# Kernel tuning notes

Measured on AMD Instinct MI355X. Metric: run time of the kernel, lower is better.

## Reference

```python
import jax, jax.numpy as jnp
import numpy as np

WS = 7           # window side
N = WS * WS      # tokens per window = 49
DIM = 384
H = 12
HD = DIM // H    # 32
BW = 2048        # num_windows * batch
NW = 4           # windows per image (mask batch)
SCALE = 1.0 / float(np.sqrt(HD))


def _rel_index():
    coords = np.stack(np.meshgrid(np.arange(WS), np.arange(WS), indexing='ij'))  # (2,7,7)
    flat = coords.reshape(2, -1)                      # (2,49)
    rel = flat[:, :, None] - flat[:, None, :]         # (2,49,49)
    rel = rel.transpose(1, 2, 0).copy()               # (49,49,2)
    rel[..., 0] += WS - 1
    rel[..., 1] += WS - 1
    rel[..., 0] *= 2 * WS - 1
    return jnp.asarray(rel.sum(-1), dtype=jnp.int32)  # (49,49)


def setup_inputs() -> dict:
    key = jax.random.key(0)
    ks = jax.random.split(key, 16)
    f32 = jnp.float32
    se = jax.random.normal(ks[0], (BW, N, DIM), dtype=f32)
    de = jax.random.normal(ks[1], (BW, N, DIM), dtype=f32)
    mask = jnp.where(jax.random.uniform(ks[2], (NW, N, N)) < 0.1, f32(-1e9), f32(0.0))
    s = 0.02
    w_v_se = jax.random.normal(ks[3], (DIM, DIM), dtype=f32) * s
    b_v_se = jnp.zeros((DIM,), dtype=f32)
    w_qkv = jax.random.normal(ks[4], (3 * DIM, DIM), dtype=f32) * s
    b_qkv = jnp.zeros((3 * DIM,), dtype=f32)
    w_proj_se = jax.random.normal(ks[5], (DIM, DIM), dtype=f32) * s
    b_proj_se = jnp.zeros((DIM,), dtype=f32)
    w_proj_de = jax.random.normal(ks[6], (DIM, DIM), dtype=f32) * s
    b_proj_de = jnp.zeros((DIM,), dtype=f32)
    rpb = jax.random.normal(ks[7], ((2 * WS - 1) ** 2, H), dtype=f32) * s  # (169,12)
    rel_idx = _rel_index()
    return {
        'se': se, 'de': de, 'mask': mask,
        'w_v_se': w_v_se, 'b_v_se': b_v_se,
        'w_qkv': w_qkv, 'b_qkv': b_qkv,
        'w_proj_se': w_proj_se, 'b_proj_se': b_proj_se,
        'w_proj_de': w_proj_de, 'b_proj_de': b_proj_de,
        'rpb': rpb, 'rel_idx': rel_idx,
    }


def reference(se, de, mask, w_v_se, b_v_se, w_qkv, b_qkv,
              w_proj_se, b_proj_se, w_proj_de, b_proj_de, rpb, rel_idx):
    B_, N_, C = se.shape
    # qkv from de (coa=False branch)
    qkv = (de @ w_qkv.T + b_qkv).reshape(B_, N_, 3, H, HD).transpose(2, 0, 3, 1, 4)
    q, k, v_de = qkv[0], qkv[1], qkv[2]                 # (B_,H,N,HD)
    v_se = (se @ w_v_se.T + b_v_se).reshape(B_, N_, H, HD).transpose(0, 2, 1, 3)
    attn = jnp.einsum('bhnd,bhmd->bhnm', q * SCALE, k)  # (B_,H,N,N)
    bias = rpb[rel_idx].transpose(2, 0, 1)              # (H,N,N)
    attn = attn + bias[None]
    # add window mask: view as (B, nW, H, N, N)
    attn = attn.reshape(B_ // NW, NW, H, N_, N_) + mask[None, :, None]
    attn = jax.nn.softmax(attn.reshape(B_, H, N_, N_), axis=-1)
    se_o = jnp.einsum('bhnm,bhmd->bnhd', attn, v_se).reshape(B_, N_, C)
    de_o = jnp.einsum('bhnm,bhmd->bnhd', attn, v_de).reshape(B_, N_, C)
    se_o = se_o @ w_proj_se.T + b_proj_se
    de_o = de_o @ w_proj_de.T + b_proj_de
    return (se_o, de_o)
```

## Files before the change

### kernel.cpp

```cpp
#include <hip/hip_runtime.h>

typedef _Float16 f16;
typedef __attribute__((ext_vector_type(8))) _Float16 f16x8;
typedef __attribute__((ext_vector_type(4))) _Float16 f16x4;
typedef __attribute__((ext_vector_type(4))) float f32x4;

#define MFMA16(a, b, c) __builtin_amdgcn_mfma_f32_16x16x32_f16(a, b, c, 0, 0, 0)

#define SCALE_F 0.17677669529663687f
#define NHEAD 12
#define NTOK 49
#define NBW 2048

__global__ void cast_f32_to_f16(const float* __restrict__ in, f16* __restrict__ out, int n4) {
    int i0 = blockIdx.x * 256 + threadIdx.x;
    int stride = gridDim.x * 256;
    for (int i = i0; i < n4; i += stride) {
        f32x4 v = ((const f32x4*)in)[i];
        f16x4 o;
#pragma unroll
        for (int e = 0; e < 4; ++e) o[e] = (f16)v[e];
        ((f16x4*)out)[i] = o;
    }
}

__global__ void prep_bm(const float* __restrict__ rpb, const int* __restrict__ rel_idx,
                        const float* __restrict__ mask, float* __restrict__ bm) {
    int blk = blockIdx.x;
    int w4 = blk / NHEAD, h = blk - w4 * NHEAD;
    for (int idx = threadIdx.x; idx < 4096; idx += 64) {
        int r = idx >> 6, c = idx & 63;
        float v = -1e30f;
        if (r < NTOK && c < NTOK)
            v = rpb[rel_idx[r * NTOK + c] * NHEAD + h] + mask[(w4 * NTOK + r) * NTOK + c];
        bm[(size_t)blk * 4096 + idx] = v;
    }
}

template <typename OUT_T>
__global__ __launch_bounds__(256) void gemm_bt(const f16* __restrict__ A, const f16* __restrict__ B,
                                               const float* __restrict__ bias, OUT_T* __restrict__ C,
                                               int M, int N, int K) {
    __shared__ __align__(16) f16 As[128 * 64];
    __shared__ __align__(16) f16 Bs[128 * 64];
    const int m0 = blockIdx.y * 128, n0 = blockIdx.x * 128;
    const int tid = threadIdx.x;
    const int w = tid >> 6, l = tid & 63;
    const int wm = w >> 1, wn = w & 1;
    const int lr = l & 15, lg = l >> 4;
    const int sp = l & 7;

    f32x4 acc[4][4] = {};

    for (int k0 = 0; k0 < K; k0 += 64) {
        __syncthreads();
#pragma unroll
        for (int it = 0; it < 4; ++it) {
            int row = w * 32 + it * 8 + (l >> 3);
            int gchunk = sp ^ (row & 7);
            const f16* gA = A + (size_t)(m0 + row) * K + k0 + gchunk * 8;
            const f16* gB = B + (size_t)(n0 + row) * K + k0 + gchunk * 8;
            f16* lA = As + (w * 32 + it * 8) * 64;
            f16* lB = Bs + (w * 32 + it * 8) * 64;
            __builtin_amdgcn_global_load_lds((const __attribute__((address_space(1))) void*)gA,
                                             (__attribute__((address_space(3))) void*)lA, 16, 0, 0);
            __builtin_amdgcn_global_load_lds((const __attribute__((address_space(1))) void*)gB,
                                             (__attribute__((address_space(3))) void*)lB, 16, 0, 0);
        }
        __syncthreads();
#pragma unroll
        for (int ks = 0; ks < 2; ++ks) {
            f16x8 af[4], bfr[4];
#pragma unroll
            for (int mi = 0; mi < 4; ++mi) {
                int r = 64 * wm + 16 * mi + lr;
                int chunk = (lg + 4 * ks) ^ (r & 7);
                af[mi] = *(const f16x8*)(As + r * 64 + chunk * 8);
            }
#pragma unroll
            for (int ni = 0; ni < 4; ++ni) {
                int r = 64 * wn + 16 * ni + lr;
                int chunk = (lg + 4 * ks) ^ (r & 7);
                bfr[ni] = *(const f16x8*)(Bs + r * 64 + chunk * 8);
            }
#pragma unroll
            for (int mi = 0; mi < 4; ++mi)
#pragma unroll
                for (int ni = 0; ni < 4; ++ni)
                    acc[mi][ni] = MFMA16(af[mi], bfr[ni], acc[mi][ni]);
        }
    }
#pragma unroll
    for (int mi = 0; mi < 4; ++mi) {
#pragma unroll
        for (int ni = 0; ni < 4; ++ni) {
            int col = n0 + 64 * wn + 16 * ni + lr;
            float bv = bias[col];
#pragma unroll
            for (int reg = 0; reg < 4; ++reg) {
                int row = m0 + 64 * wm + 16 * mi + 4 * lg + reg;
                C[(size_t)row * N + col] = (OUT_T)(acc[mi][ni][reg] + bv);
            }
        }
    }
}

__global__ __launch_bounds__(64) void attn_kernel(const f16* __restrict__ qkv,
                                                  const f16* __restrict__ vse,
                                                  const float* __restrict__ bm_all,
                                                  f16* __restrict__ att_se, f16* __restrict__ att_de) {
    __shared__ __align__(16) f16 Vts[2][32 * 64];
    __shared__ __align__(16) f16 Ps[64 * 64];

    const int bh = blockIdx.x;
    const int b = bh / NHEAD, h = bh - b * NHEAD;
    const int l = threadIdx.x;
    const int lr = l & 15, lg = l >> 4;
    const size_t wbase = (size_t)b * NTOK;

    for (int idx = l; idx < 2 * NTOK * 4; idx += 64) {
        int s = idx >= NTOK * 4;
        int t = idx - s * NTOK * 4;
        int j = t >> 2, part = t & 3;
        const f16* src = s ? (qkv + (wbase + j) * 1152 + 768 + h * 32 + part * 8)
                           : (vse + (wbase + j) * 384 + h * 32 + part * 8);
        f16x8 v = *(const f16x8*)src;
#pragma unroll
        for (int e = 0; e < 8; ++e) {
            int d = part * 8 + e;
            Vts[s][(d << 6) + (j ^ ((d & 7) << 3))] = v[e];
        }
    }
    for (int idx = l; idx < 2 * 32 * 15; idx += 64) {
        int s = idx / 480;
        int t = idx - s * 480;
        int d = t / 15, j = NTOK + (t - d * 15);
        Vts[s][(d << 6) + (j ^ ((d & 7) << 3))] = (f16)0.f;
    }

    const size_t MAXROW = (size_t)NBW * NTOK - 1;
    f16x8 qa[4], kb[4];
#pragma unroll
    for (int mi = 0; mi < 4; ++mi) {
        size_t gi = wbase + 16 * mi + lr;
        if (gi > MAXROW) gi = MAXROW;
        qa[mi] = *(const f16x8*)(qkv + gi * 1152 + h * 32 + lg * 8);
    }
#pragma unroll
    for (int ni = 0; ni < 4; ++ni) {
        size_t gj = wbase + 16 * ni + lr;
        if (gj > MAXROW) gj = MAXROW;
        kb[ni] = *(const f16x8*)(qkv + gj * 1152 + 384 + h * 32 + lg * 8);
    }
    const f32x4 zero4 = {0.f, 0.f, 0.f, 0.f};
    f32x4 S[4][4];
#pragma unroll
    for (int mi = 0; mi < 4; ++mi)
#pragma unroll
        for (int ni = 0; ni < 4; ++ni)
            S[mi][ni] = MFMA16(qa[mi], kb[ni], zero4);

    const float* bmp = bm_all + (size_t)((b & 3) * NHEAD + h) * 4096;
#pragma unroll
    for (int mi = 0; mi < 4; ++mi) {
#pragma unroll
        for (int reg = 0; reg < 4; ++reg) {
            int r = 16 * mi + 4 * lg + reg;
            float v[4];
#pragma unroll
            for (int ni = 0; ni < 4; ++ni)
                v[ni] = S[mi][ni][reg] * SCALE_F + bmp[(r << 6) + 16 * ni + lr];
            float mx = fmaxf(fmaxf(v[0], v[1]), fmaxf(v[2], v[3]));
#pragma unroll
            for (int off = 1; off < 16; off <<= 1) mx = fmaxf(mx, __shfl_xor(mx, off));
            float e[4];
            float sm = 0.f;
#pragma unroll
            for (int ni = 0; ni < 4; ++ni) {
                e[ni] = __expf(v[ni] - mx);
                sm += e[ni];
            }
#pragma unroll
            for (int off = 1; off < 16; off <<= 1) sm += __shfl_xor(sm, off);
            float inv = 1.f / sm;
#pragma unroll
            for (int ni = 0; ni < 4; ++ni)
                Ps[(r << 6) + ((16 * ni + lr) ^ ((r & 7) << 3))] = (f16)(e[ni] * inv);
        }
    }
    __syncthreads();

    f32x4 o[2][4][2] = {};
#pragma unroll
    for (int ks = 0; ks < 2; ++ks) {
        f16x8 pa[4];
#pragma unroll
        for (int mi = 0; mi < 4; ++mi) {
            int r = 16 * mi + lr;
            pa[mi] = *(const f16x8*)(Ps + (r << 6) + ((8 * lg + 32 * ks) ^ ((r & 7) << 3)));
        }
#pragma unroll
        for (int s = 0; s < 2; ++s) {
#pragma unroll
            for (int ni = 0; ni < 2; ++ni) {
                int d = 16 * ni + lr;
                f16x8 vb = *(const f16x8*)(Vts[s] + (d << 6) + ((8 * lg + 32 * ks) ^ ((d & 7) << 3)));
#pragma unroll
                for (int mi = 0; mi < 4; ++mi) o[s][mi][ni] = MFMA16(pa[mi], vb, o[s][mi][ni]);
            }
        }
    }
#pragma unroll
    for (int s = 0; s < 2; ++s) {
        f16* dst = s ? att_de : att_se;
#pragma unroll
        for (int mi = 0; mi < 4; ++mi) {
#pragma unroll
            for (int reg = 0; reg < 4; ++reg) {
                int r = 16 * mi + 4 * lg + reg;
                if (r < NTOK) {
#pragma unroll
                    for (int ni = 0; ni < 2; ++ni)
                        dst[(wbase + r) * 384 + h * 32 + 16 * ni + lr] = (f16)o[s][mi][ni][reg];
                }
            }
        }
    }
}

extern "C" void kernel_launch(void* const* d_in, const int* in_sizes, int n_in,
                              void* d_out, int out_size, void* d_ws, size_t ws_size,
                              hipStream_t stream) {
    const float* se = (const float*)d_in[0];
    const float* de = (const float*)d_in[1];
    const float* mask = (const float*)d_in[2];
    const float* w_v_se = (const float*)d_in[3];
    const float* b_v_se = (const float*)d_in[4];
    const float* w_qkv = (const float*)d_in[5];
    const float* b_qkv = (const float*)d_in[6];
    const float* w_proj_se = (const float*)d_in[7];
    const float* b_proj_se = (const float*)d_in[8];
    const float* w_proj_de = (const float*)d_in[9];
    const float* b_proj_de = (const float*)d_in[10];
    const float* rpb = (const float*)d_in[11];
    const int* rel_idx = (const int*)d_in[12];

    const size_t SE_ELEMS = (size_t)NBW * NTOK * 384;

    char* ws = (char*)d_ws;
    f16* de_h = (f16*)(ws);
    f16* se_h = (f16*)(ws + 77070336);
    f16* qkv_h = (f16*)(ws + 154140672);
    f16* vse_h = (f16*)(ws + 385351680);
    f16* wqkv_h = (f16*)(ws + 462422016);
    f16* wvse_h = (f16*)(ws + 463306752);
    f16* wpse_h = (f16*)(ws + 463601664);
    f16* wpde_h = (f16*)(ws + 463896576);
    float* bm = (float*)(ws + 464191488);

    auto cast = [&](const float* in, f16* out, size_t n) {
        int n4 = (int)(n / 4);
        int blocks = (n4 + 255) / 256;
        if (blocks > 2048) blocks = 2048;
        cast_f32_to_f16<<<blocks, 256, 0, stream>>>(in, out, n4);
    };
    cast(de, de_h, SE_ELEMS);
    cast(se, se_h, SE_ELEMS);
    cast(w_qkv, wqkv_h, (size_t)1152 * 384);
    cast(w_v_se, wvse_h, (size_t)384 * 384);
    cast(w_proj_se, wpse_h, (size_t)384 * 384);
    cast(w_proj_de, wpde_h, (size_t)384 * 384);

    prep_bm<<<48, 64, 0, stream>>>(rpb, rel_idx, mask, bm);

    gemm_bt<f16><<<dim3(9, 784), 256, 0, stream>>>(de_h, wqkv_h, b_qkv, qkv_h, 100352, 1152, 384);
    gemm_bt<f16><<<dim3(3, 784), 256, 0, stream>>>(se_h, wvse_h, b_v_se, vse_h, 100352, 384, 384);

    attn_kernel<<<NBW * NHEAD, 64, 0, stream>>>(qkv_h, vse_h, bm, de_h, se_h);

    gemm_bt<float><<<dim3(3, 784), 256, 0, stream>>>(de_h, wpse_h, b_proj_se, (float*)d_out, 100352, 384, 384);
    gemm_bt<float><<<dim3(3, 784), 256, 0, stream>>>(se_h, wpde_h, b_proj_de, (float*)d_out + SE_ELEMS, 100352,
                                                     384, 384);
}
```

Before: 724.3 us.

## Read V directly from global in attention and remap GEMM workgroups

The attention kernel no longer stages and transposes both V matrices into LDS. Instead each lane gathers its V fragment with eight strided 2-byte global loads right before the PV MFMAs, which removes the LDS transpose-and-pad pass and its shared memory. The change also drops the row clamping on Q/K loads, adds s_setprio around the MFMA bursts, and permutes the GEMM block index so consecutive blocks spread across 8 groups, for better cache locality. The costs are uncoalesced scalar global loads for V. Padding rows 49–63 now read the next window's data, or memory past the buffer for the last window, and rely on zeroed probabilities to cancel them, which is unsafe if those values are NaN or Inf.

```diff
diff --git a/kernel.cpp b/kernel.cpp
--- a/kernel.cpp
+++ b/kernel.cpp
@@ -43,7 +43,10 @@
                                                int M, int N, int K) {
     __shared__ __align__(16) f16 As[128 * 64];
     __shared__ __align__(16) f16 Bs[128 * 64];
-    const int m0 = blockIdx.y * 128, n0 = blockIdx.x * 128;
+    const int nwg = gridDim.x * gridDim.y;
+    int wg = blockIdx.y * gridDim.x + blockIdx.x;
+    wg = (wg & 7) * (nwg >> 3) + (wg >> 3);
+    const int m0 = (wg / gridDim.x) * 128, n0 = (wg % gridDim.x) * 128;
     const int tid = threadIdx.x;
     const int w = tid >> 6, l = tid & 63;
     const int wm = w >> 1, wn = w & 1;
@@ -109,7 +112,6 @@
                                                   const f16* __restrict__ vse,
                                                   const float* __restrict__ bm_all,
                                                   f16* __restrict__ att_se, f16* __restrict__ att_de) {
-    __shared__ __align__(16) f16 Vts[2][32 * 64];
     __shared__ __align__(16) f16 Ps[64 * 64];
 
     const int bh = blockIdx.x;
@@ -118,47 +120,23 @@
     const int lr = l & 15, lg = l >> 4;
     const size_t wbase = (size_t)b * NTOK;
 
-    for (int idx = l; idx < 2 * NTOK * 4; idx += 64) {
-        int s = idx >= NTOK * 4;
-        int t = idx - s * NTOK * 4;
-        int j = t >> 2, part = t & 3;
-        const f16* src = s ? (qkv + (wbase + j) * 1152 + 768 + h * 32 + part * 8)
-                           : (vse + (wbase + j) * 384 + h * 32 + part * 8);
-        f16x8 v = *(const f16x8*)src;
-#pragma unroll
-        for (int e = 0; e < 8; ++e) {
-            int d = part * 8 + e;
-            Vts[s][(d << 6) + (j ^ ((d & 7) << 3))] = v[e];
-        }
-    }
-    for (int idx = l; idx < 2 * 32 * 15; idx += 64) {
-        int s = idx / 480;
-        int t = idx - s * 480;
-        int d = t / 15, j = NTOK + (t - d * 15);
-        Vts[s][(d << 6) + (j ^ ((d & 7) << 3))] = (f16)0.f;
-    }
-
-    const size_t MAXROW = (size_t)NBW * NTOK - 1;
     f16x8 qa[4], kb[4];
 #pragma unroll
-    for (int mi = 0; mi < 4; ++mi) {
-        size_t gi = wbase + 16 * mi + lr;
-        if (gi > MAXROW) gi = MAXROW;
-        qa[mi] = *(const f16x8*)(qkv + gi * 1152 + h * 32 + lg * 8);
-    }
-#pragma unroll
-    for (int ni = 0; ni < 4; ++ni) {
-        size_t gj = wbase + 16 * ni + lr;
-        if (gj > MAXROW) gj = MAXROW;
-        kb[ni] = *(const f16x8*)(qkv + gj * 1152 + 384 + h * 32 + lg * 8);
-    }
+    for (int mi = 0; mi < 4; ++mi)
+        qa[mi] = *(const f16x8*)(qkv + (wbase + 16 * mi + lr) * 1152 + h * 32 + lg * 8);
+#pragma unroll
+    for (int ni = 0; ni < 4; ++ni)
+        kb[ni] = *(const f16x8*)(qkv + (wbase + 16 * ni + lr) * 1152 + 384 + h * 32 + lg * 8);
+
     const f32x4 zero4 = {0.f, 0.f, 0.f, 0.f};
     f32x4 S[4][4];
+    __builtin_amdgcn_s_setprio(1);
 #pragma unroll
     for (int mi = 0; mi < 4; ++mi)
 #pragma unroll
         for (int ni = 0; ni < 4; ++ni)
             S[mi][ni] = MFMA16(qa[mi], kb[ni], zero4);
+    __builtin_amdgcn_s_setprio(0);
 
     const float* bmp = bm_all + (size_t)((b & 3) * NHEAD + h) * 4096;
 #pragma unroll
@@ -190,28 +168,31 @@
     }
     __syncthreads();
 
-    f32x4 o[2][4][2] = {};
-#pragma unroll
-    for (int ks = 0; ks < 2; ++ks) {
-        f16x8 pa[4];
-#pragma unroll
-        for (int mi = 0; mi < 4; ++mi) {
-            int r = 16 * mi + lr;
-            pa[mi] = *(const f16x8*)(Ps + (r << 6) + ((8 * lg + 32 * ks) ^ ((r & 7) << 3)));
-        }
-#pragma unroll
-        for (int s = 0; s < 2; ++s) {
+#pragma unroll
+    for (int s = 0; s < 2; ++s) {
+        const f16* vbase = s ? (qkv + wbase * 1152 + 768 + h * 32) : (vse + wbase * 384 + h * 32);
+        const int RS = s ? 1152 : 384;
+        f32x4 o[4][2] = {};
+#pragma unroll
+        for (int ks = 0; ks < 2; ++ks) {
+            f16x8 pa[4];
+#pragma unroll
+            for (int mi = 0; mi < 4; ++mi) {
+                int r = 16 * mi + lr;
+                pa[mi] = *(const f16x8*)(Ps + (r << 6) + ((8 * lg + 32 * ks) ^ ((r & 7) << 3)));
+            }
 #pragma unroll
             for (int ni = 0; ni < 2; ++ni) {
-                int d = 16 * ni + lr;
-                f16x8 vb = *(const f16x8*)(Vts[s] + (d << 6) + ((8 * lg + 32 * ks) ^ ((d & 7) << 3)));
-#pragma unroll
-                for (int mi = 0; mi < 4; ++mi) o[s][mi][ni] = MFMA16(pa[mi], vb, o[s][mi][ni]);
-            }
-        }
-    }
-#pragma unroll
-    for (int s = 0; s < 2; ++s) {
+                const f16* p = vbase + (size_t)(8 * lg + 32 * ks) * RS + 16 * ni + lr;
+                f16x8 vb;
+#pragma unroll
+                for (int e = 0; e < 8; ++e) vb[e] = p[(size_t)e * RS];
+                __builtin_amdgcn_s_setprio(1);
+#pragma unroll
+                for (int mi = 0; mi < 4; ++mi) o[mi][ni] = MFMA16(pa[mi], vb, o[mi][ni]);
+                __builtin_amdgcn_s_setprio(0);
+            }
+        }
         f16* dst = s ? att_de : att_se;
 #pragma unroll
         for (int mi = 0; mi < 4; ++mi) {
@@ -221,7 +202,7 @@
                 if (r < NTOK) {
 #pragma unroll
                     for (int ni = 0; ni < 2; ++ni)
-                        dst[(wbase + r) * 384 + h * 32 + 16 * ni + lr] = (f16)o[s][mi][ni][reg];
+                        dst[(wbase + r) * 384 + h * 32 + 16 * ni + lr] = (f16)o[mi][ni][reg];
                 }
             }
         }
```

After: 681.8 us. 1.06x faster.
